# Kernel optimization log

Hardware: AMD Instinct MI355X
Metric: run time of the kernel (lower is better)

## Reference

```python
import jax, jax.numpy as jnp
import numpy as np

B, CIN, COUT, L = 8, 128, 128, 128
SCALE = 0.1


def _complex_mul(ar, ai, br, bi):
    return ar * br - ai * bi, ar * bi + ai * br


def _split_links(links):
    # links: (B, 4, L, L) -> (ux_r, ux_i, uy_r, uy_i) each (B, L, L)
    return links[:, 0], links[:, 1], links[:, 2], links[:, 3]


def _transport_forward(fr, fi, links, mu):
    ux_r, ux_i, uy_r, uy_i = _split_links(links)
    lr, li = (ux_r, ux_i) if mu == 0 else (uy_r, uy_i)
    # shift feature by -1 along spatial axis mu (axis mu+2 of (B,C,L,L))
    sr = jnp.roll(fr, shift=-1, axis=mu + 2)
    si = jnp.roll(fi, shift=-1, axis=mu + 2)
    return _complex_mul(lr[:, None], li[:, None], sr, si)


def _transport_backward(fr, fi, links, mu):
    ux_r, ux_i, uy_r, uy_i = _split_links(links)
    lr, li = (ux_r, ux_i) if mu == 0 else (uy_r, uy_i)
    cr, ci = lr, -li  # complex conjugate
    # roll conj link by +1 along its spatial axis mu (axis mu+1 of (B,L,L))
    cr = jnp.roll(cr, shift=1, axis=mu + 1)
    ci = jnp.roll(ci, shift=1, axis=mu + 1)
    sr = jnp.roll(fr, shift=1, axis=mu + 2)
    si = jnp.roll(fi, shift=1, axis=mu + 2)
    return _complex_mul(cr[:, None], ci[:, None], sr, si)


def setup_inputs() -> dict:
    key = jax.random.key(0)
    k1, k2, k3, k4, k5, k6 = jax.random.split(key, 6)
    feature_r = jax.random.normal(k1, (B, CIN, L, L), dtype=jnp.float32)
    feature_i = jax.random.normal(k2, (B, CIN, L, L), dtype=jnp.float32)
    links = jax.random.normal(k3, (B, 4, L, L), dtype=jnp.float32)
    center = SCALE * jax.random.normal(k4, (COUT, CIN), dtype=jnp.float32)
    forward_weight = SCALE * jax.random.normal(k5, (2, COUT, CIN), dtype=jnp.float32)
    backward_weight = SCALE * jax.random.normal(k6, (2, COUT, CIN), dtype=jnp.float32)
    return {
        "feature_r": feature_r,
        "feature_i": feature_i,
        "links": links,
        "center": center,
        "forward_weight": forward_weight,
        "backward_weight": backward_weight,
    }


def reference(feature_r, feature_i, links, center, forward_weight, backward_weight):
    mix = lambda w, x: jnp.einsum("oi,bixy->boxy", w, x)
    out_r = mix(center, feature_r)
    out_i = mix(center, feature_i)
    for mu in range(2):
        fwd_r, fwd_i = _transport_forward(feature_r, feature_i, links, mu)
        bwd_r, bwd_i = _transport_backward(feature_r, feature_i, links, mu)
        out_r = out_r + mix(forward_weight[mu], fwd_r) + mix(backward_weight[mu], bwd_r)
        out_i = out_i + mix(forward_weight[mu], fwd_i) + mix(backward_weight[mu], bwd_i)
    return out_r, out_i
```

## Files before the change

kernel.cpp:

```cpp
#include <hip/hip_runtime.h>
#include <stdint.h>


#define LL    128
#define NCIN  128
#define NCOUT 128
#define NB    8

typedef __attribute__((ext_vector_type(8)))  __bf16 bf16x8;
typedef __attribute__((ext_vector_type(4)))  __bf16 bf16x4;
typedef __attribute__((ext_vector_type(16))) float  f32x16;
typedef __attribute__((ext_vector_type(4)))  float  f32x4;

#define FEAT_BYTES 98304
#define WROW 40
#define W_BYTES (5 * 128 * WROW * 2)
#define LDS_BYTES (FEAT_BYTES + W_BYTES)

__global__ __launch_bounds__(512, 2)
void lconv_kernel(const float* __restrict__ frg, const float* __restrict__ fig,
                  const float* __restrict__ links, const float* __restrict__ wc,
                  const float* __restrict__ wf, const float* __restrict__ wb,
                  float* __restrict__ out)
{
    extern __shared__ char smem[];
    float*  feat = (float*)smem;
    __bf16* wlds = (__bf16*)(smem + FEAT_BYTES);

    const int tid  = threadIdx.x;
    const int lane = tid & 63;
    const int wv   = tid >> 6;
    const int l5   = lane >> 5;
    const int ln   = lane & 31;
    const int Mrow = wv >> 2;
    const int Ncol = wv & 3;

    const int bid     = blockIdx.x;
    const int logical = (bid & 7) * 128 + (bid >> 3);
    const int b = logical >> 7;
    const int x = logical & 127;
    const int xm = (x + 127) & 127;

    const int y  = Ncol * 32 + ln;
    const int yp = (y + 1) & 127;
    const int ym = (y + 127) & 127;

    const float* Lb = links + (size_t)b * 4 * LL * LL;
    const float lr1 =  Lb[(0*LL + x )*LL + y ];
    const float li1 =  Lb[(1*LL + x )*LL + y ];
    const float lr2 =  Lb[(0*LL + xm)*LL + y ];
    const float li2 = -Lb[(1*LL + xm)*LL + y ];
    const float lr3 =  Lb[(2*LL + x )*LL + y ];
    const float li3 =  Lb[(3*LL + x )*LL + y ];
    const float lr4 =  Lb[(2*LL + x )*LL + ym];
    const float li4 = -Lb[(3*LL + x )*LL + ym];

    f32x16 accR0 = {}, accR1 = {}, accI0 = {}, accI1 = {};

    for (int kc = 0; kc < 4; ++kc) {
        if (kc > 0) __syncthreads();

        #pragma unroll
        for (int j = 0; j < 12; ++j) {
            const int q    = tid + j * 512;
            const int idx  = q * 4;
            const int irow = idx >> 7;
            const int y0   = idx & 127;
            const int comp = (irow >= 96) ? 1 : 0;
            const int rr   = irow - comp * 96;
            const int row  = rr >> 5;
            const int io   = rr & 31;
            const int xs   = (x + row + 127) & 127;
            const float* g = (comp ? fig : frg)
                + (((size_t)b * NCIN + (size_t)(kc * 32 + io)) * LL + xs) * LL + y0;
            *(f32x4*)(feat + idx) = *(const f32x4*)g;
        }

        #pragma unroll
        for (int j = 0; j < 10; ++j) {
            const int dd = j >> 1;
            const float* wsd = (dd == 0) ? wc
                             : (dd == 1) ? wf
                             : (dd == 2) ? wb
                             : (dd == 3) ? (wf + NCOUT * NCIN)
                                         : (wb + NCOUT * NCIN);
            const int r  = (j & 1) * 512 + tid;
            const int o  = r >> 3;
            const int k4 = (r & 7) * 4;
            const f32x4 w4 = *(const f32x4*)(wsd + o * NCIN + kc * 32 + k4);
            bf16x4 h;
            h[0] = (__bf16)w4.x; h[1] = (__bf16)w4.y;
            h[2] = (__bf16)w4.z; h[3] = (__bf16)w4.w;
            *(bf16x4*)&wlds[(dd * 128 + o) * WROW + k4] = h;
        }

        __syncthreads();

        #pragma unroll
        for (int d = 0; d < 5; ++d) {
            const int   row_d = (d == 1) ? 2 : (d == 2) ? 0 : 1;
            const int   ysrc  = (d == 3) ? yp : (d == 4) ? ym : y;
            const float lr    = (d == 1) ? lr1 : (d == 2) ? lr2 : (d == 3) ? lr3
                              : (d == 4) ? lr4 : 1.0f;
            const float li    = (d == 1) ? li1 : (d == 2) ? li2 : (d == 3) ? li3
                              : (d == 4) ? li4 : 0.0f;

            const int fbr = row_d * 4096 + ysrc;
            const int fbi = 12288 + row_d * 4096 + ysrc;

            #pragma unroll
            for (int kk = 0; kk < 2; ++kk) {
                const int ib = kk * 16 + 8 * l5;
                float fr8[8], fi8[8];
                #pragma unroll
                for (int j = 0; j < 8; ++j) fr8[j] = feat[fbr + (ib + j) * 128];
                #pragma unroll
                for (int j = 0; j < 8; ++j) fi8[j] = feat[fbi + (ib + j) * 128];

                bf16x8 Br, Bi;
                #pragma unroll
                for (int j = 0; j < 8; ++j) {
                    float br, bi2;
                    if (d == 0) { br = fr8[j]; bi2 = fi8[j]; }
                    else        { br  = lr * fr8[j] - li * fi8[j];
                                  bi2 = lr * fi8[j] + li * fr8[j]; }
                    Br[j] = (__bf16)br;
                    Bi[j] = (__bf16)bi2;
                }

                #pragma unroll
                for (int mt = 0; mt < 2; ++mt) {
                    const int oo = (d * 128 + Mrow * 64 + mt * 32 + ln) * WROW
                                 + kk * 16 + 8 * l5;
                    const bf16x8 A = *(const bf16x8*)&wlds[oo];
                    f32x16& aR = mt ? accR1 : accR0;
                    f32x16& aI = mt ? accI1 : accI0;
                    aR = __builtin_amdgcn_mfma_f32_32x32x16_bf16(A, Br, aR, 0, 0, 0);
                    aI = __builtin_amdgcn_mfma_f32_32x32x16_bf16(A, Bi, aI, 0, 0, 0);
                }
            }
        }
    }

    const size_t OFF = (size_t)NB * NCOUT * LL * LL;
    #pragma unroll
    for (int mt = 0; mt < 2; ++mt) {
        const f32x16 aR = mt ? accR1 : accR0;
        const f32x16 aI = mt ? accI1 : accI0;
        const int ob = Mrow * 64 + mt * 32 + 4 * l5;
        #pragma unroll
        for (int r = 0; r < 16; ++r) {
            const int o = ob + (r & 3) + 8 * (r >> 2);
            const size_t idx = (((size_t)(b * NCOUT + o)) * LL + x) * LL + y;
            __builtin_nontemporal_store(aR[r], &out[idx]);
            __builtin_nontemporal_store(aI[r], &out[OFF + idx]);
        }
    }
}

extern "C" void kernel_launch(void* const* d_in, const int* in_sizes, int n_in,
                              void* d_out, int out_size, void* d_ws, size_t ws_size,
                              hipStream_t stream) {
    (void)in_sizes; (void)n_in; (void)out_size; (void)d_ws; (void)ws_size;
    const float* frg   = (const float*)d_in[0];
    const float* fig   = (const float*)d_in[1];
    const float* links = (const float*)d_in[2];
    const float* wc    = (const float*)d_in[3];
    const float* wf    = (const float*)d_in[4];
    const float* wb    = (const float*)d_in[5];
    float* out = (float*)d_out;

    hipFuncSetAttribute((const void*)lconv_kernel,
                        hipFuncAttributeMaxDynamicSharedMemorySize, LDS_BYTES);

    lconv_kernel<<<dim3(1024), dim3(512), LDS_BYTES, stream>>>(
        frg, fig, links, wc, wf, wb, out);
}
```

Baseline: 311.3 us.

## Pack real/imag features as bf16 pairs in a padded LDS layout

Feature staging now converts real and imaginary fp32 values to bf16 at load time and packs them into one 32-bit word per element. The LDS tile is stored in a padded blocked layout (132-dword blocks) so each B-fragment read takes one LDS load instead of two. This halves the LDS footprint and read traffic, which may allow higher occupancy. The cost is an earlier rounding of features to bf16, before the complex multiply by the link, which adds a little precision loss, plus extra pack/unpack bit operations.

Result: no change. 305.7 us (-1.8%).

```diff
diff --git a/kernel.cpp b/kernel.cpp
--- a/kernel.cpp
+++ b/kernel.cpp
@@ -11,11 +11,21 @@
 typedef __attribute__((ext_vector_type(4)))  __bf16 bf16x4;
 typedef __attribute__((ext_vector_type(16))) float  f32x16;
 typedef __attribute__((ext_vector_type(4)))  float  f32x4;
-
-#define FEAT_BYTES 98304
-#define WROW 40
-#define W_BYTES (5 * 128 * WROW * 2)
-#define LDS_BYTES (FEAT_BYTES + W_BYTES)
+typedef __attribute__((ext_vector_type(4)))  uint32_t u32x4;
+
+#define FP_BLOCK 132
+#define FP_ROW   (32 * FP_BLOCK)
+#define FP_DW    (3 * FP_ROW)
+#define WROW     40
+#define W_BYTES  (5 * 128 * WROW * 2)
+#define LDS_BYTES (FP_DW * 4 + W_BYTES)
+
+__device__ __forceinline__ float pair_lo_f32(uint32_t p) {
+    uint32_t v = p << 16; return __builtin_bit_cast(float, v);
+}
+__device__ __forceinline__ float pair_hi_f32(uint32_t p) {
+    uint32_t v = p & 0xFFFF0000u; return __builtin_bit_cast(float, v);
+}
 
 __global__ __launch_bounds__(512, 2)
 void lconv_kernel(const float* __restrict__ frg, const float* __restrict__ fig,
@@ -24,8 +34,8 @@
                   float* __restrict__ out)
 {
     extern __shared__ char smem[];
-    float*  feat = (float*)smem;
-    __bf16* wlds = (__bf16*)(smem + FEAT_BYTES);
+    uint32_t* fp   = (uint32_t*)smem;
+    __bf16*   wlds = (__bf16*)(smem + FP_DW * 4);
 
     const int tid  = threadIdx.x;
     const int lane = tid & 63;
@@ -61,19 +71,25 @@
         if (kc > 0) __syncthreads();
 
         #pragma unroll
-        for (int j = 0; j < 12; ++j) {
-            const int q    = tid + j * 512;
-            const int idx  = q * 4;
-            const int irow = idx >> 7;
-            const int y0   = idx & 127;
-            const int comp = (irow >= 96) ? 1 : 0;
-            const int rr   = irow - comp * 96;
-            const int row  = rr >> 5;
-            const int io   = rr & 31;
-            const int xs   = (x + row + 127) & 127;
-            const float* g = (comp ? fig : frg)
-                + (((size_t)b * NCIN + (size_t)(kc * 32 + io)) * LL + xs) * LL + y0;
-            *(f32x4*)(feat + idx) = *(const f32x4*)g;
+        for (int j = 0; j < 6; ++j) {
+            const int g   = tid + j * 512;
+            const int row = g >> 10;
+            const int rem = g & 1023;
+            const int io  = rem >> 5;
+            const int yb  = rem & 31;
+            const int xs  = (x + row + 127) & 127;
+            const size_t ga = (((size_t)(b * NCIN + kc * 32 + io)) * LL + xs) * LL
+                            + (size_t)(yb * 4);
+            const f32x4 fr4 = *(const f32x4*)(frg + ga);
+            const f32x4 fi4 = *(const f32x4*)(fig + ga);
+            u32x4 pk;
+            #pragma unroll
+            for (int v = 0; v < 4; ++v) {
+                const uint32_t lo = (uint32_t)__builtin_bit_cast(uint16_t, (__bf16)fr4[v]);
+                const uint32_t hi = (uint32_t)__builtin_bit_cast(uint16_t, (__bf16)fi4[v]);
+                pk[v] = (hi << 16) | lo;
+            }
+            *(u32x4*)(fp + row * FP_ROW + yb * FP_BLOCK + io * 4) = pk;
         }
 
         #pragma unroll
@@ -105,27 +121,34 @@
             const float li    = (d == 1) ? li1 : (d == 2) ? li2 : (d == 3) ? li3
                               : (d == 4) ? li4 : 0.0f;
 
-            const int fbr = row_d * 4096 + ysrc;
-            const int fbi = 12288 + row_d * 4096 + ysrc;
+            const int base = row_d * FP_ROW + (ysrc >> 2) * FP_BLOCK + (ysrc & 3);
 
             #pragma unroll
             for (int kk = 0; kk < 2; ++kk) {
                 const int ib = kk * 16 + 8 * l5;
-                float fr8[8], fi8[8];
+                uint32_t p[8];
                 #pragma unroll
-                for (int j = 0; j < 8; ++j) fr8[j] = feat[fbr + (ib + j) * 128];
-                #pragma unroll
-                for (int j = 0; j < 8; ++j) fi8[j] = feat[fbi + (ib + j) * 128];
+                for (int j = 0; j < 8; ++j)
+                    p[j] = fp[base + (ib + j) * 4];
 
                 bf16x8 Br, Bi;
-                #pragma unroll
-                for (int j = 0; j < 8; ++j) {
-                    float br, bi2;
-                    if (d == 0) { br = fr8[j]; bi2 = fi8[j]; }
-                    else        { br  = lr * fr8[j] - li * fi8[j];
-                                  bi2 = lr * fi8[j] + li * fr8[j]; }
-                    Br[j] = (__bf16)br;
-                    Bi[j] = (__bf16)bi2;
+                if (d == 0) {
+                    u32x4 br, bi;
+                    #pragma unroll
+                    for (int q = 0; q < 4; ++q) {
+                        br[q] = (p[2*q] & 0xFFFFu) | (p[2*q+1] << 16);
+                        bi[q] = (p[2*q] >> 16)     | (p[2*q+1] & 0xFFFF0000u);
+                    }
+                    Br = __builtin_bit_cast(bf16x8, br);
+                    Bi = __builtin_bit_cast(bf16x8, bi);
+                } else {
+                    #pragma unroll
+                    for (int j = 0; j < 8; ++j) {
+                        const float fr = pair_lo_f32(p[j]);
+                        const float fi = pair_hi_f32(p[j]);
+                        Br[j] = (__bf16)(lr * fr - li * fi);
+                        Bi[j] = (__bf16)(lr * fi + li * fr);
+                    }
                 }
 
                 #pragma unroll
```
